# Optimization experiments

Hardware: AMD Instinct MI355X
Metric: run time of the kernel (lower is better)

## Reference

```python
import jax, jax.numpy as jnp
import numpy as np

GROUPS = 32
EPS = 1e-6


def group_norm(x, gamma, beta):
    b, h, w, c = x.shape
    xg = x.reshape(b, h, w, GROUPS, c // GROUPS)
    mean = jnp.mean(xg, axis=(1, 2, 4), keepdims=True)
    var = jnp.var(xg, axis=(1, 2, 4), keepdims=True)
    xg = (xg - mean) * jax.lax.rsqrt(var + EPS)
    return xg.reshape(b, h, w, c) * gamma + beta


def setup_inputs() -> dict:
    key = jax.random.key(0)
    ks = jax.random.split(key, 6)
    B, H, W, C = 4, 64, 64, 512
    scale = 0.02
    return {
        "x": jax.random.normal(ks[0], (B, H, W, C), dtype=jnp.float32),
        "gamma": jnp.ones((C,), dtype=jnp.float32),
        "beta": jnp.zeros((C,), dtype=jnp.float32),
        "wq": jax.random.normal(ks[1], (C, C), dtype=jnp.float32) * scale,
        "bq": jnp.zeros((C,), dtype=jnp.float32),
        "wk": jax.random.normal(ks[2], (C, C), dtype=jnp.float32) * scale,
        "bk": jnp.zeros((C,), dtype=jnp.float32),
        "wv": jax.random.normal(ks[3], (C, C), dtype=jnp.float32) * scale,
        "bv": jnp.zeros((C,), dtype=jnp.float32),
        "wo": jax.random.normal(ks[4], (C, C), dtype=jnp.float32) * scale,
        "bo": jnp.zeros((C,), dtype=jnp.float32),
    }


def reference(x, gamma, beta, wq, bq, wk, bk, wv, bv, wo, bo):
    b, h, w, c = x.shape
    xn = group_norm(x, gamma, beta)
    # 1x1 convs == per-pixel linear layers
    q = (jnp.einsum('bhwc,cd->bhwd', xn, wq) + bq).reshape(b, h * w, c)
    k = (jnp.einsum('bhwc,cd->bhwd', xn, wk) + bk).reshape(b, h * w, c)
    v = (jnp.einsum('bhwc,cd->bhwd', xn, wv) + bv).reshape(b, h * w, c)
    # full (hw x hw) attention, single head
    scores = jnp.einsum('bic,bjc->bij', q, k) * (c ** -0.5)  # [b, hw, hw]
    attn = jax.nn.softmax(scores, axis=-1)
    out = jnp.einsum('bij,bjc->bic', attn, v).reshape(b, h, w, c)
    return jnp.einsum('bhwc,cd->bhwd', out, wo) + bo + x
```

## Files before the change

kernel.cpp:

```cpp
#include <hip/hip_runtime.h>
#include <stdint.h>


typedef __attribute__((ext_vector_type(8))) short bf16x8;
typedef __attribute__((ext_vector_type(8))) unsigned short u16x8;
typedef __attribute__((ext_vector_type(4))) float f32x4;

#define QSCALE_LOG2E 0.06376435229f

__device__ __forceinline__ unsigned short f2bf(float f) {
  unsigned int x = __float_as_uint(f);
  x += 0x7fffu + ((x >> 16) & 1u);
  return (unsigned short)(x >> 16);
}
__device__ __forceinline__ float bf2f(unsigned short u) {
  return __uint_as_float((unsigned int)u << 16);
}

__device__ __forceinline__ void gl_lds16(const void* g, void* l) {
  __builtin_amdgcn_global_load_lds(
      (__attribute__((address_space(1))) unsigned char*)g,
      (__attribute__((address_space(3))) unsigned char*)l, 16, 0, 0);
}

__device__ __forceinline__ void gemm_tile(
    const unsigned short* __restrict__ A, long lda,
    const unsigned short* __restrict__ B, long ldb,
    int K, unsigned short* As, unsigned short* Bs, f32x4 acc[4][4]) {
  const int tid = threadIdx.x;
  const int wave = tid >> 6, lane = tid & 63;
  const int srow = lane >> 3;
  const int soff = ((lane & 7) ^ srow) * 16;
  const int wm = (wave >> 1) * 64, wn = (wave & 1) * 64;
  const int lrow = lane & 15;
  const int rsw = lrow & 7;
  const int kgb = lane >> 4;

  for (int k0 = 0; k0 < K; k0 += 64) {
    __syncthreads();
    for (int i = 0; i < 4; ++i) {
      int chunk = wave * 4 + i;
      int row = chunk * 8 + srow;
      gl_lds16((const char*)(A + (long)row * lda + k0) + soff, (char*)As + chunk * 1024);
      gl_lds16((const char*)(B + (long)row * ldb + k0) + soff, (char*)Bs + chunk * 1024);
    }
    __syncthreads();
#pragma unroll
    for (int ks = 0; ks < 2; ++ks) {
      bf16x8 af[4], bfr[4];
      const int off = ((ks * 4 + kgb) ^ rsw) * 8;
#pragma unroll
      for (int t = 0; t < 4; ++t) {
        af[t]  = *(const bf16x8*)&As[(wm + t * 16 + lrow) * 64 + off];
        bfr[t] = *(const bf16x8*)&Bs[(wn + t * 16 + lrow) * 64 + off];
      }
#pragma unroll
      for (int mt = 0; mt < 4; ++mt)
#pragma unroll
        for (int nt = 0; nt < 4; ++nt)
          acc[mt][nt] = __builtin_amdgcn_mfma_f32_16x16x32_bf16(af[mt], bfr[nt], acc[mt][nt], 0, 0, 0);
    }
  }
}

#define EPILOG_SETUP                                          \
  const int lane = threadIdx.x & 63, wave = threadIdx.x >> 6; \
  const int wm = (wave >> 1) * 64, wn = (wave & 1) * 64;      \
  const int lcol = lane & 15, lrb = (lane >> 4) * 4;

__global__ __launch_bounds__(256) void prep_gn_kernel(
    const float* __restrict__ x, float* __restrict__ stats,
    const float* __restrict__ wq, const float* __restrict__ wk,
    const float* __restrict__ wv, const float* __restrict__ wo,
    const float* __restrict__ bq, const float* __restrict__ bk,
    const float* __restrict__ bv,
    unsigned short* __restrict__ wqkvT, unsigned short* __restrict__ woT,
    float* __restrict__ bias) {
  const int tid = threadIdx.x;
  if (blockIdx.x < 512) {
    const int b = blockIdx.x >> 7, slab = blockIdx.x & 127;
    const float* xp = x + (long)b * 4096 * 512 + (long)slab * 32 * 512;
    float s = 0.f, s2 = 0.f;
    for (int it = 0; it < 16; ++it) {
      int i = it * 256 + tid;
      float4 v = *(const float4*)(xp + (long)i * 4);
      s += v.x + v.y + v.z + v.w;
      s2 += v.x * v.x + v.y * v.y + v.z * v.z + v.w * v.w;
    }
    s += __shfl_xor(s, 1); s += __shfl_xor(s, 2);
    s2 += __shfl_xor(s2, 1); s2 += __shfl_xor(s2, 2);
    if ((tid & 3) == 0) {
      int g = (tid & 127) >> 2;
      atomicAdd(&stats[(b * 32 + g) * 2], s);
      atomicAdd(&stats[(b * 32 + g) * 2 + 1], s2);
    }
    return;
  }
  long id = (long)(blockIdx.x - 512) * 256 + tid;
  if (id < 786432) {
    long n = id >> 9, k = id & 511;
    const float* w = (n < 512) ? wq : (n < 1024 ? wk : wv);
    wqkvT[id] = f2bf(w[k * 512 + (n & 511)]);
  } else if (id < 786432 + 262144) {
    long j = id - 786432, n = j >> 9, k = j & 511;
    woT[j] = f2bf(wo[k * 512 + n]);
  } else if (id < 786432 + 262144 + 1536) {
    long j = id - 786432 - 262144;
    bias[j] = (j < 512) ? bq[j] : (j < 1024 ? bk[j - 512] : bv[j - 1024]);
  }
}

__global__ __launch_bounds__(256) void gn_apply(const float* __restrict__ x,
                                                const float* __restrict__ stats,
                                                const float* __restrict__ gamma,
                                                const float* __restrict__ beta,
                                                unsigned short* __restrict__ xn) {
  long id = (long)blockIdx.x * 256 + threadIdx.x;
  long a = id * 4;
  int b = (int)(id >> 19);
  int ch = (int)(a & 511);
  int g = ch >> 4;
  float s = stats[(b * 32 + g) * 2], s2 = stats[(b * 32 + g) * 2 + 1];
  float mean = s * (1.f / 65536.f);
  float rinv = rsqrtf(s2 * (1.f / 65536.f) - mean * mean + 1e-6f);
  float4 v = *(const float4*)(x + a);
  float4 gm = *(const float4*)(gamma + ch);
  float4 bt = *(const float4*)(beta + ch);
  ushort4 o;
  o.x = f2bf((v.x - mean) * rinv * gm.x + bt.x);
  o.y = f2bf((v.y - mean) * rinv * gm.y + bt.y);
  o.z = f2bf((v.z - mean) * rinv * gm.z + bt.z);
  o.w = f2bf((v.w - mean) * rinv * gm.w + bt.w);
  *(ushort4*)(xn + a) = o;
}

__global__ __launch_bounds__(256) void qkv_kernel(
    const unsigned short* __restrict__ xn, const unsigned short* __restrict__ wqkvT,
    const float* __restrict__ bias, unsigned short* __restrict__ q,
    unsigned short* __restrict__ kk, unsigned short* __restrict__ vv) {
  __shared__ unsigned short As[128 * 64], Bs[128 * 64];
  f32x4 acc[4][4] = {};
  const long tm = (long)blockIdx.x * 128, tn = (long)blockIdx.y * 128;
  gemm_tile(xn + tm * 512, 512, wqkvT + tn * 512, 512, 512, As, Bs, acc);
  EPILOG_SETUP
  const int sel = blockIdx.y >> 2;
  unsigned short* outp = (sel == 0) ? q : (sel == 1) ? kk : vv;
  const float scale = (sel == 0) ? QSCALE_LOG2E : 1.f;
  const long nloc0 = tn - (long)sel * 512;
#pragma unroll
  for (int mt = 0; mt < 4; ++mt)
#pragma unroll
    for (int nt = 0; nt < 4; ++nt)
#pragma unroll
      for (int r = 0; r < 4; ++r) {
        long m = tm + wm + mt * 16 + lrb + r;
        long ng = tn + wn + nt * 16 + lcol;
        float v = (acc[mt][nt][r] + bias[ng]) * scale;
        outp[m * 512 + (nloc0 + wn + nt * 16 + lcol)] = f2bf(v);
      }
}

__global__ __launch_bounds__(256) void transpose_v(const unsigned short* __restrict__ v,
                                                   unsigned short* __restrict__ vT) {
  const int b = blockIdx.z;
  const long j0 = (long)blockIdx.x * 64, c0 = (long)blockIdx.y * 64;
  __shared__ unsigned short t[64][72];
  const int tc = (threadIdx.x & 15) * 4, tr = threadIdx.x >> 4;
  for (int rr = 0; rr < 64; rr += 16) {
    ushort4 u = *(const ushort4*)&v[((long)b * 4096 + j0 + tr + rr) * 512 + c0 + tc];
    t[tr + rr][tc] = u.x; t[tr + rr][tc + 1] = u.y;
    t[tr + rr][tc + 2] = u.z; t[tr + rr][tc + 3] = u.w;
  }
  __syncthreads();
  for (int rr = 0; rr < 64; rr += 16) {
    int c = tr + rr;
    ushort4 o;
    o.x = t[tc + 0][c]; o.y = t[tc + 1][c]; o.z = t[tc + 2][c]; o.w = t[tc + 3][c];
    *(ushort4*)&vT[((long)b * 512 + c0 + c) * 4096 + j0 + tc] = o;
  }
}

__global__ __launch_bounds__(256) void qkt_kernel(
    const unsigned short* __restrict__ q, const unsigned short* __restrict__ kk,
    unsigned short* __restrict__ probs, float* __restrict__ lsum, int b0) {
  __shared__ unsigned short As[128 * 64], Bs[128 * 64];
  f32x4 acc[4][4] = {};
  const int z = blockIdx.z;
  const long bb = (long)(b0 + z) * 4096 * 512;
  const long tm = (long)blockIdx.x * 128, tn = (long)blockIdx.y * 128;
  gemm_tile(q + bb + tm * 512, 512, kk + bb + tn * 512, 512, 512, As, Bs, acc);
  EPILOG_SETUP
  unsigned short* out = probs + (long)z * 4096 * 4096;
  float* ls = lsum + (long)(b0 + z) * 4096;
#pragma unroll
  for (int mt = 0; mt < 4; ++mt) {
    float rsum[4] = {0.f, 0.f, 0.f, 0.f};
#pragma unroll
    for (int nt = 0; nt < 4; ++nt)
#pragma unroll
      for (int r = 0; r < 4; ++r) {
        long m = tm + wm + mt * 16 + lrb + r;
        long n = tn + wn + nt * 16 + lcol;
        float e = exp2f(acc[mt][nt][r]);
        out[m * 4096 + n] = f2bf(e);
        rsum[r] += e;
      }
#pragma unroll
    for (int r = 0; r < 4; ++r) {
      float s = rsum[r];
      s += __shfl_xor(s, 1); s += __shfl_xor(s, 2);
      s += __shfl_xor(s, 4); s += __shfl_xor(s, 8);
      if (lcol == 0) atomicAdd(&ls[tm + wm + mt * 16 + lrb + r], s);
    }
  }
}

__global__ __launch_bounds__(256) void pv_kernel(
    const unsigned short* __restrict__ probs, const unsigned short* __restrict__ vT,
    unsigned short* __restrict__ part, int b0) {
  __shared__ unsigned short As[128 * 64], Bs[128 * 64];
  f32x4 acc[4][4] = {};
  const int zb = blockIdx.z >> 2, s = blockIdx.z & 3;
  const long tm = (long)blockIdx.x * 128, tn = (long)blockIdx.y * 128;
  gemm_tile(probs + (long)zb * 4096 * 4096 + tm * 4096 + s * 1024, 4096,
            vT + (long)(b0 + zb) * 512 * 4096 + tn * 4096 + s * 1024, 4096,
            1024, As, Bs, acc);
  EPILOG_SETUP
  unsigned short* out = part + (long)blockIdx.z * 4096 * 512;
#pragma unroll
  for (int mt = 0; mt < 4; ++mt)
#pragma unroll
    for (int nt = 0; nt < 4; ++nt)
#pragma unroll
      for (int r = 0; r < 4; ++r) {
        long m = tm + wm + mt * 16 + lrb + r;
        long n = tn + wn + nt * 16 + lcol;
        out[m * 512 + n] = f2bf(acc[mt][nt][r]);
      }
}

__global__ __launch_bounds__(256) void reduce_kernel(const unsigned short* __restrict__ part,
                                                     const float* __restrict__ lsum,
                                                     unsigned short* __restrict__ attn,
                                                     int b0) {
  const long elems = 4096l * 512;
  const int zb = blockIdx.y;
  const unsigned short* pp = part + (long)zb * 4 * elems;
  long id = (long)blockIdx.x * 256 + threadIdx.x;
  long a = id * 8;
  int m = (int)(a >> 9);
  float inv = 1.f / lsum[(long)(b0 + zb) * 4096 + m];
  u16x8 p0 = *(const u16x8*)(pp + a);
  u16x8 p1 = *(const u16x8*)(pp + elems + a);
  u16x8 p2 = *(const u16x8*)(pp + 2 * elems + a);
  u16x8 p3 = *(const u16x8*)(pp + 3 * elems + a);
  u16x8 o;
#pragma unroll
  for (int j = 0; j < 8; ++j)
    o[j] = f2bf((bf2f(p0[j]) + bf2f(p1[j]) + bf2f(p2[j]) + bf2f(p3[j])) * inv);
  *(u16x8*)(attn + (long)(b0 + zb) * elems + a) = o;
}

__global__ __launch_bounds__(256) void proj_kernel(
    const unsigned short* __restrict__ attn, const unsigned short* __restrict__ woT,
    const float* __restrict__ bo, const float* __restrict__ x,
    float* __restrict__ out) {
  __shared__ unsigned short As[128 * 64], Bs[128 * 64];
  f32x4 acc[4][4] = {};
  const long tm = (long)blockIdx.x * 128, tn = (long)blockIdx.y * 128;
  gemm_tile(attn + tm * 512, 512, woT + tn * 512, 512, 512, As, Bs, acc);
  EPILOG_SETUP
#pragma unroll
  for (int mt = 0; mt < 4; ++mt)
#pragma unroll
    for (int nt = 0; nt < 4; ++nt)
#pragma unroll
      for (int r = 0; r < 4; ++r) {
        long m = tm + wm + mt * 16 + lrb + r;
        long n = tn + wn + nt * 16 + lcol;
        out[m * 512 + n] = acc[mt][nt][r] + bo[n] + x[m * 512 + n];
      }
}

extern "C" void kernel_launch(void* const* d_in, const int* in_sizes, int n_in,
                              void* d_out, int out_size, void* d_ws, size_t ws_size,
                              hipStream_t stream) {
  const float* x     = (const float*)d_in[0];
  const float* gamma = (const float*)d_in[1];
  const float* beta  = (const float*)d_in[2];
  const float* wq    = (const float*)d_in[3];
  const float* bq    = (const float*)d_in[4];
  const float* wk    = (const float*)d_in[5];
  const float* bk    = (const float*)d_in[6];
  const float* wv    = (const float*)d_in[7];
  const float* bv    = (const float*)d_in[8];
  const float* wo    = (const float*)d_in[9];
  const float* bo    = (const float*)d_in[10];

  char* p = (char*)d_ws;
  auto take = [&](size_t bytes) { char* r = p; p += (bytes + 255) & ~(size_t)255; return r; };
  const long NTOK = 16384, C = 512, HW = 4096;
  unsigned short* xn    = (unsigned short*)take(NTOK * C * 2);
  unsigned short* q     = (unsigned short*)take(NTOK * C * 2);
  unsigned short* kbuf  = (unsigned short*)take(NTOK * C * 2);
  unsigned short* vT    = (unsigned short*)take(NTOK * C * 2);
  unsigned short* wqkvT = (unsigned short*)take(1536l * 512 * 2);
  unsigned short* woT   = (unsigned short*)take(512l * 512 * 2);
  float* bias           = (float*)take(1536 * 4);
  float* stats          = (float*)take(256 * 4);
  float* lsum           = (float*)take(16384 * 4);

  size_t fixed = (size_t)(p - (char*)d_ws);
  size_t per_nb = (size_t)HW * HW * 2 + 4ul * HW * C * 2 + 512;
  int NB = (ws_size >= fixed + 4 * per_nb) ? 4
         : (ws_size >= fixed + 2 * per_nb) ? 2 : 1;
  unsigned short* probs = (unsigned short*)take((size_t)NB * HW * HW * 2);
  unsigned short* part  = (unsigned short*)take((size_t)NB * 4 * HW * C * 2);
  unsigned short* attn  = xn;
  unsigned short* vbuf  = part;

  hipMemsetAsync(stats, 0, (size_t)((char*)(lsum + 16384) - (char*)stats), stream);
  prep_gn_kernel<<<512 + 4103, 256, 0, stream>>>(x, stats, wq, wk, wv, wo,
                                                 bq, bk, bv, wqkvT, woT, bias);
  gn_apply<<<8192, 256, 0, stream>>>(x, stats, gamma, beta, xn);

  qkv_kernel<<<dim3(128, 12), 256, 0, stream>>>(xn, wqkvT, bias, q, kbuf, vbuf);
  transpose_v<<<dim3(64, 8, 4), 256, 0, stream>>>(vbuf, vT);

  for (int b0 = 0; b0 < 4; b0 += NB) {
    qkt_kernel<<<dim3(32, 32, NB), 256, 0, stream>>>(q, kbuf, probs, lsum, b0);
    pv_kernel<<<dim3(32, 4, 4 * NB), 256, 0, stream>>>(probs, vT, part, b0);
    reduce_kernel<<<dim3(1024, NB), 256, 0, stream>>>(part, lsum, attn, b0);
  }

  proj_kernel<<<dim3(128, 4), 256, 0, stream>>>(attn, woT, bo, x, (float*)d_out);
}
```

Measured before the change: 426.3 us.

## Stage GEMM epilogues through LDS for vectorized coalesced global stores

Result: no change. 418.9 us (-1.7%).

```diff
diff --git a/kernel.cpp b/kernel.cpp
--- a/kernel.cpp
+++ b/kernel.cpp
@@ -138,26 +138,34 @@
     const unsigned short* __restrict__ xn, const unsigned short* __restrict__ wqkvT,
     const float* __restrict__ bias, unsigned short* __restrict__ q,
     unsigned short* __restrict__ kk, unsigned short* __restrict__ vv) {
-  __shared__ unsigned short As[128 * 64], Bs[128 * 64];
+  __shared__ __align__(16) unsigned short sbuf[16384];
   f32x4 acc[4][4] = {};
   const long tm = (long)blockIdx.x * 128, tn = (long)blockIdx.y * 128;
-  gemm_tile(xn + tm * 512, 512, wqkvT + tn * 512, 512, 512, As, Bs, acc);
+  gemm_tile(xn + tm * 512, 512, wqkvT + tn * 512, 512, 512, sbuf, sbuf + 8192, acc);
   EPILOG_SETUP
   const int sel = blockIdx.y >> 2;
   unsigned short* outp = (sel == 0) ? q : (sel == 1) ? kk : vv;
   const float scale = (sel == 0) ? QSCALE_LOG2E : 1.f;
   const long nloc0 = tn - (long)sel * 512;
-#pragma unroll
-  for (int mt = 0; mt < 4; ++mt)
-#pragma unroll
-    for (int nt = 0; nt < 4; ++nt)
-#pragma unroll
-      for (int r = 0; r < 4; ++r) {
-        long m = tm + wm + mt * 16 + lrb + r;
-        long ng = tn + wn + nt * 16 + lcol;
-        float v = (acc[mt][nt][r] + bias[ng]) * scale;
-        outp[m * 512 + (nloc0 + wn + nt * 16 + lcol)] = f2bf(v);
-      }
+  __syncthreads();
+  unsigned short* wbuf = sbuf + wave * 2176;
+#pragma unroll
+  for (int mt = 0; mt < 4; ++mt) {
+#pragma unroll
+    for (int nt = 0; nt < 4; ++nt) {
+      float bn = bias[tn + wn + nt * 16 + lcol];
+#pragma unroll
+      for (int r = 0; r < 4; ++r)
+        wbuf[(lrb + r) * 68 + nt * 16 + lcol] = f2bf((acc[mt][nt][r] + bn) * scale);
+    }
+#pragma unroll
+    for (int i = 0; i < 2; ++i) {
+      int chunk = lane + 64 * i;
+      int row = chunk >> 3, c8 = chunk & 7;
+      u16x8 vvv = *(const u16x8*)&wbuf[row * 68 + c8 * 8];
+      *(u16x8*)&outp[(tm + wm + mt * 16 + row) * 512 + nloc0 + wn + c8 * 8] = vvv;
+    }
+  }
 }
 
 __global__ __launch_bounds__(256) void transpose_v(const unsigned short* __restrict__ v,
@@ -183,60 +191,74 @@
 __global__ __launch_bounds__(256) void qkt_kernel(
     const unsigned short* __restrict__ q, const unsigned short* __restrict__ kk,
     unsigned short* __restrict__ probs, float* __restrict__ lsum, int b0) {
-  __shared__ unsigned short As[128 * 64], Bs[128 * 64];
+  __shared__ __align__(16) unsigned short sbuf[16384];
   f32x4 acc[4][4] = {};
   const int z = blockIdx.z;
   const long bb = (long)(b0 + z) * 4096 * 512;
   const long tm = (long)blockIdx.x * 128, tn = (long)blockIdx.y * 128;
-  gemm_tile(q + bb + tm * 512, 512, kk + bb + tn * 512, 512, 512, As, Bs, acc);
+  gemm_tile(q + bb + tm * 512, 512, kk + bb + tn * 512, 512, 512, sbuf, sbuf + 8192, acc);
   EPILOG_SETUP
   unsigned short* out = probs + (long)z * 4096 * 4096;
   float* ls = lsum + (long)(b0 + z) * 4096;
+  __syncthreads();
+  unsigned short* wbuf = sbuf + wave * 2176;
 #pragma unroll
   for (int mt = 0; mt < 4; ++mt) {
-    float rsum[4] = {0.f, 0.f, 0.f, 0.f};
+    float rs[4] = {0.f, 0.f, 0.f, 0.f};
 #pragma unroll
     for (int nt = 0; nt < 4; ++nt)
 #pragma unroll
       for (int r = 0; r < 4; ++r) {
-        long m = tm + wm + mt * 16 + lrb + r;
-        long n = tn + wn + nt * 16 + lcol;
         float e = exp2f(acc[mt][nt][r]);
-        out[m * 4096 + n] = f2bf(e);
-        rsum[r] += e;
+        rs[r] += e;
+        wbuf[(lrb + r) * 68 + nt * 16 + lcol] = f2bf(e);
       }
 #pragma unroll
     for (int r = 0; r < 4; ++r) {
-      float s = rsum[r];
+      float s = rs[r];
       s += __shfl_xor(s, 1); s += __shfl_xor(s, 2);
       s += __shfl_xor(s, 4); s += __shfl_xor(s, 8);
       if (lcol == 0) atomicAdd(&ls[tm + wm + mt * 16 + lrb + r], s);
     }
+#pragma unroll
+    for (int i = 0; i < 2; ++i) {
+      int chunk = lane + 64 * i;
+      int row = chunk >> 3, c8 = chunk & 7;
+      u16x8 vvv = *(const u16x8*)&wbuf[row * 68 + c8 * 8];
+      *(u16x8*)&out[(tm + wm + mt * 16 + row) * 4096 + tn + wn + c8 * 8] = vvv;
+    }
   }
 }
 
 __global__ __launch_bounds__(256) void pv_kernel(
     const unsigned short* __restrict__ probs, const unsigned short* __restrict__ vT,
     unsigned short* __restrict__ part, int b0) {
-  __shared__ unsigned short As[128 * 64], Bs[128 * 64];
+  __shared__ __align__(16) unsigned short sbuf[16384];
   f32x4 acc[4][4] = {};
   const int zb = blockIdx.z >> 2, s = blockIdx.z & 3;
   const long tm = (long)blockIdx.x * 128, tn = (long)blockIdx.y * 128;
   gemm_tile(probs + (long)zb * 4096 * 4096 + tm * 4096 + s * 1024, 4096,
             vT + (long)(b0 + zb) * 512 * 4096 + tn * 4096 + s * 1024, 4096,
-            1024, As, Bs, acc);
+            1024, sbuf, sbuf + 8192, acc);
   EPILOG_SETUP
   unsigned short* out = part + (long)blockIdx.z * 4096 * 512;
-#pragma unroll
-  for (int mt = 0; mt < 4; ++mt)
+  __syncthreads();
+  unsigned short* wbuf = sbuf + wave * 2176;
+#pragma unroll
+  for (int mt = 0; mt < 4; ++mt) {
 #pragma unroll
     for (int nt = 0; nt < 4; ++nt)
 #pragma unroll
-      for (int r = 0; r < 4; ++r) {
-        long m = tm + wm + mt * 16 + lrb + r;
-        long n = tn + wn + nt * 16 + lcol;
-        out[m * 512 + n] = f2bf(acc[mt][nt][r]);
-      }
+      for (int r = 0; r < 4; ++r)
+        wbuf[(lrb + r) * 68 + nt * 16 + lcol] = f2bf(acc[mt][nt][r]);
+#pragma unroll
+    for (int i = 0; i < 2; ++i) {
+      int chunk = lane + 64 * i;
+      int row = chunk >> 3, c8 = chunk & 7;
+      u16x8 vvv = *(const u16x8*)&wbuf[row * 68 + c8 * 8];
+      *(u16x8*)&out[(tm + wm + mt * 16 + row) * 512 + tn + wn + c8 * 8] = vvv;
+    }
+  }
 }
 
 __global__ __launch_bounds__(256) void reduce_kernel(const unsigned short* __restrict__ part,
@@ -265,21 +287,34 @@
     const unsigned short* __restrict__ attn, const unsigned short* __restrict__ woT,
     const float* __restrict__ bo, const float* __restrict__ x,
     float* __restrict__ out) {
-  __shared__ unsigned short As[128 * 64], Bs[128 * 64];
+  __shared__ __align__(16) unsigned short sbuf[16384];
   f32x4 acc[4][4] = {};
   const long tm = (long)blockIdx.x * 128, tn = (long)blockIdx.y * 128;
-  gemm_tile(attn + tm * 512, 512, woT + tn * 512, 512, 512, As, Bs, acc);
+  gemm_tile(attn + tm * 512, 512, woT + tn * 512, 512, 512, sbuf, sbuf + 8192, acc);
   EPILOG_SETUP
-#pragma unroll
-  for (int mt = 0; mt < 4; ++mt)
-#pragma unroll
-    for (int nt = 0; nt < 4; ++nt)
-#pragma unroll
-      for (int r = 0; r < 4; ++r) {
-        long m = tm + wm + mt * 16 + lrb + r;
-        long n = tn + wn + nt * 16 + lcol;
-        out[m * 512 + n] = acc[mt][nt][r] + bo[n] + x[m * 512 + n];
-      }
+  __syncthreads();
+  float* wbuf = (float*)sbuf + wave * 1088;
+#pragma unroll
+  for (int mt = 0; mt < 4; ++mt) {
+#pragma unroll
+    for (int nt = 0; nt < 4; ++nt) {
+      float bn = bo[tn + wn + nt * 16 + lcol];
+#pragma unroll
+      for (int r = 0; r < 4; ++r)
+        wbuf[(lrb + r) * 68 + nt * 16 + lcol] = acc[mt][nt][r] + bn;
+    }
+#pragma unroll
+    for (int i = 0; i < 4; ++i) {
+      int chunk = lane + 64 * i;
+      int row = chunk >> 4, c4 = chunk & 15;
+      float4 v = *(const float4*)&wbuf[row * 68 + c4 * 4];
+      long m = tm + wm + mt * 16 + row;
+      long n0 = tn + wn + c4 * 4;
+      float4 xr = *(const float4*)&x[m * 512 + n0];
+      v.x += xr.x; v.y += xr.y; v.z += xr.z; v.w += xr.w;
+      *(float4*)&out[m * 512 + n0] = v;
+    }
+  }
 }
 
 extern "C" void kernel_launch(void* const* d_in, const int* in_sizes, int n_in,
```
